# Optimization experiments

Measured on AMD Instinct MI355X. Metric: run time of the kernel, lower is better.

Reference implementation:

```python
import jax, jax.numpy as jnp
import numpy as np

B, T, H, O = 256, 2048, 64, 2


def setup_inputs() -> dict:
    key = jax.random.key(0)
    ks = jax.random.split(key, 14)
    def lin(k, out_f, in_f):
        bound = np.sqrt(6.0 / (in_f + out_f))
        return jax.random.uniform(k, (out_f, in_f), jnp.float32, -bound, bound)
    return {
        "x": jax.random.normal(ks[0], (B, T, 2), jnp.float32),
        "h0": jax.random.normal(ks[1], (1, B, H), jnp.float32),
        "Wa": lin(ks[2], H, H + 1), "ba": jnp.zeros((H,), jnp.float32),
        "Wp1": lin(ks[3], H, H + 1), "bp1": jnp.zeros((H,), jnp.float32),
        "Wp2": lin(ks[4], H, H + 1), "bp2": jnp.zeros((H,), jnp.float32),
        "Wf": lin(ks[5], H, 2 * H), "bf": jnp.zeros((H,), jnp.float32),
        "Wg": lin(ks[6], H, 2 * H), "bg": jnp.zeros((H,), jnp.float32),
        "Wo": lin(ks[7], O, H), "bo": jnp.zeros((O,), jnp.float32),
    }


def reference(x, h0, Wa, ba, Wp1, bp1, Wp2, bp2, Wf, bf, Wg, bg, Wo, bo):
    # x: [B, T, 2] (I/Q), h0: [1, B, H]
    xt = jnp.swapaxes(x, 0, 1)  # [T, B, 2]

    def step(h, x_t):
        i = x_t[:, 0:1]
        q = x_t[:, 1:2]
        amp = jnp.sqrt(i * i + q * q)
        theta = jnp.arctan2(q, i)
        cos_t = jnp.cos(theta)
        sin_t = jnp.sin(theta)
        a = jnp.tanh(jnp.concatenate([h, amp], -1) @ Wa.T + ba)
        p1 = jnp.tanh(jnp.concatenate([h, cos_t], -1) @ Wp1.T + bp1)
        p2 = jnp.tanh(jnp.concatenate([h, sin_t], -1) @ Wp2.T + bp2)
        u = a * p1 * p2 * (1 - a) * (1 - p1) * (1 - p2)
        hu = jnp.concatenate([h, u], -1)
        f = jax.nn.sigmoid(hu @ Wf.T + bf)
        g = jnp.tanh(hu @ Wg.T + bg)
        h_new = f * h + (1 - f) * g
        y = h_new @ Wo.T + bo
        return h_new, y

    _, ys = jax.lax.scan(step, h0[0], xt)  # ys: [T, B, O]
    return jnp.swapaxes(ys, 0, 1)  # [B, T, O]
```

## Files before the change

kernel.cpp:

```cpp
#include <hip/hip_runtime.h>
#include <math.h>

#define BB 256
#define TT 2048
#define HH 64

typedef _Float16 half2v __attribute__((ext_vector_type(2)));
typedef __fp16  fp16v2 __attribute__((ext_vector_type(2)));
union H2I { half2v h; int i; };

#if __has_builtin(__builtin_amdgcn_rcpf)
__device__ __forceinline__ float fast_rcp(float v) { return __builtin_amdgcn_rcpf(v); }
#else
__device__ __forceinline__ float fast_rcp(float v) { return 1.0f / v; }
#endif
#if __has_builtin(__builtin_amdgcn_rsqf)
__device__ __forceinline__ float fast_rsq(float v) { return __builtin_amdgcn_rsqf(v); }
#else
__device__ __forceinline__ float fast_rsq(float v) { return rsqrtf(v); }
#endif

__device__ __forceinline__ float tanh_fast(float v) {
    float e = __expf(2.0f * v);
    return fmaf(-2.0f, fast_rcp(e + 1.0f), 1.0f);
}

__device__ __forceinline__ float sigmoid_fast(float v) {
    return fast_rcp(1.0f + __expf(-v));
}

__device__ __forceinline__ float fdot2(half2v a, half2v b, float c) {
    return __builtin_amdgcn_fdot2(a, b, c, false);
}

__device__ __forceinline__ half2v pack_pair(float a, float b) {
    fp16v2 r = __builtin_amdgcn_cvt_pkrtz(a, b);
    return __builtin_bit_cast(half2v, r);
}

__device__ __forceinline__ void pin_h2(half2v& v) {
    H2I u; u.h = v;
    asm volatile("" : "+v"(u.i));
    v = u.h;
}

__device__ __forceinline__ half2v bcast_pair(half2v v, int lane) {
    H2I u; u.h = v;
    H2I w; w.i = __builtin_amdgcn_readlane(u.i, lane);
    return w.h;
}

__device__ __forceinline__ float dpp_neighbor(float v) {
    return __int_as_float(__builtin_amdgcn_mov_dpp(__float_as_int(v), 0xB1, 0xf, 0xf, true));
}

template <int CTRL>
__device__ __forceinline__ float dpp_add_stage(float v) {
    int t = __builtin_amdgcn_update_dpp(0, __float_as_int(v), CTRL, 0xf, 0xf, true);
    return v + __int_as_float(t);
}

__device__ __forceinline__ float wave_sum_dpp(float v) {
    v = dpp_add_stage<0x111>(v);
    v = dpp_add_stage<0x112>(v);
    v = dpp_add_stage<0x114>(v);
    v = dpp_add_stage<0x118>(v);
    v = dpp_add_stage<0x142>(v);
    v = dpp_add_stage<0x143>(v);
    return v;
}

__global__ __launch_bounds__(256, 1)
void pgjanet_kernel(const float* __restrict__ x,
                    const float* __restrict__ h0,
                    const float* __restrict__ Wa,  const float* __restrict__ ba,
                    const float* __restrict__ Wp1, const float* __restrict__ bp1,
                    const float* __restrict__ Wp2, const float* __restrict__ bp2,
                    const float* __restrict__ Wf,  const float* __restrict__ bf,
                    const float* __restrict__ Wg,  const float* __restrict__ bg,
                    const float* __restrict__ Wo,  const float* __restrict__ bo,
                    float* __restrict__ out)
{
    const int b   = blockIdx.x;
    const int tid = threadIdx.x;
    const int j   = tid & 63;
    const int w   = __builtin_amdgcn_readfirstlane(tid >> 6);

    __shared__ float xs[TT * 2];
    __shared__ float ybuf[TT * 2];
    __shared__ float exch[2][5][HH];

    {
        const float* xp = x + (size_t)b * (TT * 2);
        for (int i = tid; i < TT * 2; i += 256) xs[i] = xp[i];
    }

    const float* gsrc  = (w == 0) ? Wa : (w == 1) ? Wp1 : (w == 2) ? Wp2 : Wf;
    const int    gld   = (w < 3) ? (HH + 1) : (2 * HH);
    const float* g2src = (w == 3) ? Wg : gsrc;
    const int    g2ld  = (w == 3) ? (2 * HH) : gld;

    half2v wgate[32], wgate2[32], wfuv[32], wguv[32];
#pragma unroll
    for (int m = 0; m < 32; ++m) {
        wgate[m]  = pack_pair(gsrc [j * gld  + 2 * m], gsrc [j * gld  + 2 * m + 1]);
        wgate2[m] = pack_pair(g2src[j * g2ld + 2 * m], g2src[j * g2ld + 2 * m + 1]);
        wfuv[m]   = pack_pair(Wf[j * (2 * HH) + HH + 2 * m], Wf[j * (2 * HH) + HH + 2 * m + 1]);
        wguv[m]   = pack_pair(Wg[j * (2 * HH) + HH + 2 * m], Wg[j * (2 * HH) + HH + 2 * m + 1]);
    }
#pragma unroll
    for (int m = 0; m < 32; ++m) {
        pin_h2(wgate[m]); pin_h2(wgate2[m]); pin_h2(wfuv[m]); pin_h2(wguv[m]);
    }

    const float xw   = (w == 0) ? Wa [j * (HH + 1) + HH]
                     : (w == 1) ? Wp1[j * (HH + 1) + HH]
                     : (w == 2) ? Wp2[j * (HH + 1) + HH] : 0.f;
    const float bsel = (w == 0) ? ba[j] : (w == 1) ? bp1[j] : (w == 2) ? bp2[j] : 0.f;
    const float bf_r = bf[j], bg_r = bg[j];
    const float wo0 = Wo[j], wo1 = Wo[HH + j];
    const float bo0 = bo[0], bo1 = bo[1];

    float h = h0[b * HH + j];
    float* yp = out + (size_t)b * (TT * 2);

    __syncthreads();

    float xsel;
    {
        float xi = xs[0], xq = xs[1];
        float r2 = xi * xi + xq * xq;
        float rsq = fast_rsq(r2);
        bool ok = r2 > 0.f;
        float amp = ok ? r2 * rsq : 0.f;
        float ct  = ok ? xi * rsq : 1.f;
        float st  = ok ? xq * rsq : 0.f;
        xsel = (w == 0) ? amp : (w == 1) ? ct : st;
    }

    for (int t = 0; t < TT; ++t) {
        float (*ex)[HH] = exch[t & 1];

        const int tn = (t + 1 < TT) ? (t + 1) : (TT - 1);
        float xi_n = xs[2 * tn], xq_n = xs[2 * tn + 1];
        float xsel_n;
        {
            float r2 = xi_n * xi_n + xq_n * xq_n;
            float rsq = fast_rsq(r2);
            bool ok = r2 > 0.f;
            float amp = ok ? r2 * rsq : 0.f;
            float ct  = ok ? xi_n * rsq : 1.f;
            float st  = ok ? xq_n * rsq : 0.f;
            xsel_n = (w == 0) ? amp : (w == 1) ? ct : st;
        }

        float hnbr = dpp_neighbor(h);
        half2v hp = pack_pair(h, hnbr);
        half2v sh[32];
#pragma unroll
        for (int m = 0; m < 32; ++m) sh[m] = bcast_pair(hp, 2 * m);

        float a0 = 0.f, a1 = 0.f, a2 = 0.f, a3 = 0.f;
#pragma unroll
        for (int m = 0; m < 8; ++m) {
            a0 = fdot2(sh[m],      wgate[m],      a0);
            a1 = fdot2(sh[m + 8],  wgate[m + 8],  a1);
            a2 = fdot2(sh[m + 16], wgate[m + 16], a2);
            a3 = fdot2(sh[m + 24], wgate[m + 24], a3);
        }
        float pre = (a0 + a1) + (a2 + a3);

        if (w == 3) {
            float b0 = 0.f, b1 = 0.f, b2 = 0.f, b3 = 0.f;
#pragma unroll
            for (int m = 0; m < 8; ++m) {
                b0 = fdot2(sh[m],      wgate2[m],      b0);
                b1 = fdot2(sh[m + 8],  wgate2[m + 8],  b1);
                b2 = fdot2(sh[m + 16], wgate2[m + 16], b2);
                b3 = fdot2(sh[m + 24], wgate2[m + 24], b3);
            }
            ex[3][j] = pre + bf_r;
            ex[4][j] = ((b0 + b1) + (b2 + b3)) + bg_r;
        } else {
            ex[w][j] = tanh_fast(pre + fmaf(xsel, xw, bsel));
        }

        __syncthreads();

        float av  = ex[0][j];
        float pv1 = ex[1][j];
        float pv2 = ex[2][j];
        float fh  = ex[3][j];
        float gh  = ex[4][j];
        float u = (av * (1.f - av)) * (pv1 * (1.f - pv1)) * (pv2 * (1.f - pv2));

        float unbr = dpp_neighbor(u);
        half2v upk = pack_pair(u, unbr);
        half2v su[32];
#pragma unroll
        for (int m = 0; m < 32; ++m) su[m] = bcast_pair(upk, 2 * m);

        float f0 = 0.f, f1 = 0.f, f2 = 0.f, f3 = 0.f;
        float g0 = 0.f, g1 = 0.f, g2 = 0.f, g3 = 0.f;
#pragma unroll
        for (int m = 0; m < 8; ++m) {
            f0 = fdot2(su[m],      wfuv[m],      f0);
            f1 = fdot2(su[m + 8],  wfuv[m + 8],  f1);
            f2 = fdot2(su[m + 16], wfuv[m + 16], f2);
            f3 = fdot2(su[m + 24], wfuv[m + 24], f3);
            g0 = fdot2(su[m],      wguv[m],      g0);
            g1 = fdot2(su[m + 8],  wguv[m + 8],  g1);
            g2 = fdot2(su[m + 16], wguv[m + 16], g2);
            g3 = fdot2(su[m + 24], wguv[m + 24], g3);
        }
        float f = sigmoid_fast(fh + (f0 + f1) + (f2 + f3));
        float g = tanh_fast(gh + (g0 + g1) + (g2 + g3));
        h = fmaf(f, h - g, g);

        if (w == (t & 3)) {
            float y0 = wave_sum_dpp(h * wo0);
            float y1 = wave_sum_dpp(h * wo1);
            if (j == 63) {
                ybuf[2 * t]     = y0 + bo0;
                ybuf[2 * t + 1] = y1 + bo1;
            }
        }

        xsel = xsel_n;
    }

    __syncthreads();
    {
        const float4* ys4 = reinterpret_cast<const float4*>(ybuf);
        float4*       yp4 = reinterpret_cast<float4*>(yp);
        for (int i = tid; i < TT * 2 / 4; i += 256) yp4[i] = ys4[i];
    }
}

extern "C" void kernel_launch(void* const* d_in, const int* in_sizes, int n_in,
                              void* d_out, int out_size, void* d_ws, size_t ws_size,
                              hipStream_t stream) {
    const float* x   = (const float*)d_in[0];
    const float* h0  = (const float*)d_in[1];
    const float* Wa  = (const float*)d_in[2];
    const float* ba  = (const float*)d_in[3];
    const float* Wp1 = (const float*)d_in[4];
    const float* bp1 = (const float*)d_in[5];
    const float* Wp2 = (const float*)d_in[6];
    const float* bp2 = (const float*)d_in[7];
    const float* Wf  = (const float*)d_in[8];
    const float* bf  = (const float*)d_in[9];
    const float* Wg  = (const float*)d_in[10];
    const float* bg  = (const float*)d_in[11];
    const float* Wo  = (const float*)d_in[12];
    const float* bo  = (const float*)d_in[13];
    float* out = (float*)d_out;

    pgjanet_kernel<<<dim3(BB), dim3(256), 0, stream>>>(
        x, h0, Wa, ba, Wp1, bp1, Wp2, bp2, Wf, bf, Wg, bg, Wo, bo, out);
}
```

Baseline: 1.511 ms.

## Collapse per-batch work into one wave and remove per-step block barriers

Each batch element now runs in a single 64-thread wave instead of four waves that split the gate matmuls and swapped results through LDS with a __syncthreads every timestep. One wave computes all five h-projections and both u-projections itself, keeping all seven weight matrices in registers. Output projections are deferred: h is buffered in LDS and every 64 steps each lane computes one timestep's outputs, writing them straight to global memory. This removes the per-step barrier and LDS exchange, but puts more serial dot-product work on each wave, with higher register pressure and less parallelism per CU.

```diff
diff --git a/kernel.cpp b/kernel.cpp
--- a/kernel.cpp
+++ b/kernel.cpp
@@ -54,23 +54,7 @@
     return __int_as_float(__builtin_amdgcn_mov_dpp(__float_as_int(v), 0xB1, 0xf, 0xf, true));
 }
 
-template <int CTRL>
-__device__ __forceinline__ float dpp_add_stage(float v) {
-    int t = __builtin_amdgcn_update_dpp(0, __float_as_int(v), CTRL, 0xf, 0xf, true);
-    return v + __int_as_float(t);
-}
-
-__device__ __forceinline__ float wave_sum_dpp(float v) {
-    v = dpp_add_stage<0x111>(v);
-    v = dpp_add_stage<0x112>(v);
-    v = dpp_add_stage<0x114>(v);
-    v = dpp_add_stage<0x118>(v);
-    v = dpp_add_stage<0x142>(v);
-    v = dpp_add_stage<0x143>(v);
-    return v;
-}
-
-__global__ __launch_bounds__(256, 1)
+__global__ __launch_bounds__(64, 1)
 void pgjanet_kernel(const float* __restrict__ x,
                     const float* __restrict__ h0,
                     const float* __restrict__ Wa,  const float* __restrict__ ba,
@@ -81,159 +65,137 @@
                     const float* __restrict__ Wo,  const float* __restrict__ bo,
                     float* __restrict__ out)
 {
-    const int b   = blockIdx.x;
-    const int tid = threadIdx.x;
-    const int j   = tid & 63;
-    const int w   = __builtin_amdgcn_readfirstlane(tid >> 6);
+    const int b = blockIdx.x;
+    const int j = threadIdx.x;
 
     __shared__ float xs[TT * 2];
-    __shared__ float ybuf[TT * 2];
-    __shared__ float exch[2][5][HH];
+    __shared__ float hbuf[64][HH + 1];
+    __shared__ float woLDS[2 * HH];
 
     {
-        const float* xp = x + (size_t)b * (TT * 2);
-        for (int i = tid; i < TT * 2; i += 256) xs[i] = xp[i];
-    }
-
-    const float* gsrc  = (w == 0) ? Wa : (w == 1) ? Wp1 : (w == 2) ? Wp2 : Wf;
-    const int    gld   = (w < 3) ? (HH + 1) : (2 * HH);
-    const float* g2src = (w == 3) ? Wg : gsrc;
-    const int    g2ld  = (w == 3) ? (2 * HH) : gld;
-
-    half2v wgate[32], wgate2[32], wfuv[32], wguv[32];
-#pragma unroll
-    for (int m = 0; m < 32; ++m) {
-        wgate[m]  = pack_pair(gsrc [j * gld  + 2 * m], gsrc [j * gld  + 2 * m + 1]);
-        wgate2[m] = pack_pair(g2src[j * g2ld + 2 * m], g2src[j * g2ld + 2 * m + 1]);
-        wfuv[m]   = pack_pair(Wf[j * (2 * HH) + HH + 2 * m], Wf[j * (2 * HH) + HH + 2 * m + 1]);
-        wguv[m]   = pack_pair(Wg[j * (2 * HH) + HH + 2 * m], Wg[j * (2 * HH) + HH + 2 * m + 1]);
-    }
-#pragma unroll
-    for (int m = 0; m < 32; ++m) {
-        pin_h2(wgate[m]); pin_h2(wgate2[m]); pin_h2(wfuv[m]); pin_h2(wguv[m]);
-    }
-
-    const float xw   = (w == 0) ? Wa [j * (HH + 1) + HH]
-                     : (w == 1) ? Wp1[j * (HH + 1) + HH]
-                     : (w == 2) ? Wp2[j * (HH + 1) + HH] : 0.f;
-    const float bsel = (w == 0) ? ba[j] : (w == 1) ? bp1[j] : (w == 2) ? bp2[j] : 0.f;
+        const float4* xp4 = reinterpret_cast<const float4*>(x + (size_t)b * (TT * 2));
+        float4*       xs4 = reinterpret_cast<float4*>(xs);
+#pragma unroll
+        for (int i = 0; i < (TT * 2 / 4) / 64; ++i) xs4[j + 64 * i] = xp4[j + 64 * i];
+    }
+    for (int i = j; i < 2 * HH; i += 64) woLDS[i] = Wo[i];
+
+    half2v w5[5][32], wfu[32], wgu[32];
+    {
+        const float* Wsrc[5] = {Wa, Wp1, Wp2, Wf, Wg};
+        const int    ldv[5]  = {HH + 1, HH + 1, HH + 1, 2 * HH, 2 * HH};
+#pragma unroll
+        for (int g = 0; g < 5; ++g) {
+            const float* r = Wsrc[g] + (size_t)j * ldv[g];
+#pragma unroll
+            for (int m = 0; m < 32; ++m) w5[g][m] = pack_pair(r[2 * m], r[2 * m + 1]);
+        }
+        const float* rf = Wf + (size_t)j * (2 * HH) + HH;
+        const float* rg = Wg + (size_t)j * (2 * HH) + HH;
+#pragma unroll
+        for (int m = 0; m < 32; ++m) {
+            wfu[m] = pack_pair(rf[2 * m], rf[2 * m + 1]);
+            wgu[m] = pack_pair(rg[2 * m], rg[2 * m + 1]);
+        }
+#pragma unroll
+        for (int g = 0; g < 5; ++g)
+#pragma unroll
+            for (int m = 0; m < 32; ++m) pin_h2(w5[g][m]);
+#pragma unroll
+        for (int m = 0; m < 32; ++m) { pin_h2(wfu[m]); pin_h2(wgu[m]); }
+    }
+
+    const float waX  = Wa [j * (HH + 1) + HH];
+    const float wp1X = Wp1[j * (HH + 1) + HH];
+    const float wp2X = Wp2[j * (HH + 1) + HH];
+    const float ba_r = ba[j], bp1_r = bp1[j], bp2_r = bp2[j];
     const float bf_r = bf[j], bg_r = bg[j];
-    const float wo0 = Wo[j], wo1 = Wo[HH + j];
-    const float bo0 = bo[0], bo1 = bo[1];
-
-    float h = h0[b * HH + j];
+    const float bo0  = bo[0], bo1 = bo[1];
+
+    float  h  = h0[b * HH + j];
     float* yp = out + (size_t)b * (TT * 2);
 
     __syncthreads();
 
-    float xsel;
+    float amp, ct, st;
     {
         float xi = xs[0], xq = xs[1];
         float r2 = xi * xi + xq * xq;
-        float rsq = fast_rsq(r2);
+        float rq = fast_rsq(r2);
         bool ok = r2 > 0.f;
-        float amp = ok ? r2 * rsq : 0.f;
-        float ct  = ok ? xi * rsq : 1.f;
-        float st  = ok ? xq * rsq : 0.f;
-        xsel = (w == 0) ? amp : (w == 1) ? ct : st;
+        amp = ok ? r2 * rq : 0.f;
+        ct  = ok ? xi * rq : 1.f;
+        st  = ok ? xq * rq : 0.f;
     }
 
     for (int t = 0; t < TT; ++t) {
-        float (*ex)[HH] = exch[t & 1];
-
-        const int tn = (t + 1 < TT) ? (t + 1) : (TT - 1);
+        const int tn = (t + 1 < TT) ? (t + 1) : t;
         float xi_n = xs[2 * tn], xq_n = xs[2 * tn + 1];
-        float xsel_n;
+        float amp_n, ct_n, st_n;
         {
             float r2 = xi_n * xi_n + xq_n * xq_n;
-            float rsq = fast_rsq(r2);
+            float rq = fast_rsq(r2);
             bool ok = r2 > 0.f;
-            float amp = ok ? r2 * rsq : 0.f;
-            float ct  = ok ? xi_n * rsq : 1.f;
-            float st  = ok ? xq_n * rsq : 0.f;
-            xsel_n = (w == 0) ? amp : (w == 1) ? ct : st;
-        }
-
-        float hnbr = dpp_neighbor(h);
-        half2v hp = pack_pair(h, hnbr);
+            amp_n = ok ? r2 * rq : 0.f;
+            ct_n  = ok ? xi_n * rq : 1.f;
+            st_n  = ok ? xq_n * rq : 0.f;
+        }
+
+        float  hnbr = dpp_neighbor(h);
+        half2v hp   = pack_pair(h, hnbr);
         half2v sh[32];
 #pragma unroll
         for (int m = 0; m < 32; ++m) sh[m] = bcast_pair(hp, 2 * m);
 
-        float a0 = 0.f, a1 = 0.f, a2 = 0.f, a3 = 0.f;
-#pragma unroll
-        for (int m = 0; m < 8; ++m) {
-            a0 = fdot2(sh[m],      wgate[m],      a0);
-            a1 = fdot2(sh[m + 8],  wgate[m + 8],  a1);
-            a2 = fdot2(sh[m + 16], wgate[m + 16], a2);
-            a3 = fdot2(sh[m + 24], wgate[m + 24], a3);
-        }
-        float pre = (a0 + a1) + (a2 + a3);
-
-        if (w == 3) {
-            float b0 = 0.f, b1 = 0.f, b2 = 0.f, b3 = 0.f;
-#pragma unroll
-            for (int m = 0; m < 8; ++m) {
-                b0 = fdot2(sh[m],      wgate2[m],      b0);
-                b1 = fdot2(sh[m + 8],  wgate2[m + 8],  b1);
-                b2 = fdot2(sh[m + 16], wgate2[m + 16], b2);
-                b3 = fdot2(sh[m + 24], wgate2[m + 24], b3);
+        float acc[5];
+        acc[0] = fmaf(amp, waX,  ba_r);
+        acc[1] = fmaf(ct,  wp1X, bp1_r);
+        acc[2] = fmaf(st,  wp2X, bp2_r);
+        acc[3] = bf_r;
+        acc[4] = bg_r;
+#pragma unroll
+        for (int m = 0; m < 32; ++m)
+#pragma unroll
+            for (int g = 0; g < 5; ++g)
+                acc[g] = fdot2(sh[m], w5[g][m], acc[g]);
+
+        float av = tanh_fast(acc[0]);
+        float p1 = tanh_fast(acc[1]);
+        float p2 = tanh_fast(acc[2]);
+        float u = fmaf(-av, av, av) * fmaf(-p1, p1, p1) * fmaf(-p2, p2, p2);
+
+        float  unbr = dpp_neighbor(u);
+        half2v up   = pack_pair(u, unbr);
+        half2v su[32];
+#pragma unroll
+        for (int m = 0; m < 32; ++m) su[m] = bcast_pair(up, 2 * m);
+
+        float f0 = acc[3], f1 = 0.f, g0 = acc[4], g1 = 0.f;
+#pragma unroll
+        for (int m = 0; m < 16; ++m) {
+            f0 = fdot2(su[m],      wfu[m],      f0);
+            f1 = fdot2(su[m + 16], wfu[m + 16], f1);
+            g0 = fdot2(su[m],      wgu[m],      g0);
+            g1 = fdot2(su[m + 16], wgu[m + 16], g1);
+        }
+        float f = sigmoid_fast(f0 + f1);
+        float g = tanh_fast(g0 + g1);
+        h = fmaf(f, h - g, g);
+
+        hbuf[t & 63][j] = h;
+
+        if ((t & 63) == 63) {
+            float y0 = bo0, y1 = bo1;
+#pragma unroll 4
+            for (int k = 0; k < HH; ++k) {
+                float hv = hbuf[j][k];
+                y0 = fmaf(hv, woLDS[k],      y0);
+                y1 = fmaf(hv, woLDS[HH + k], y1);
             }
-            ex[3][j] = pre + bf_r;
-            ex[4][j] = ((b0 + b1) + (b2 + b3)) + bg_r;
-        } else {
-            ex[w][j] = tanh_fast(pre + fmaf(xsel, xw, bsel));
-        }
-
-        __syncthreads();
-
-        float av  = ex[0][j];
-        float pv1 = ex[1][j];
-        float pv2 = ex[2][j];
-        float fh  = ex[3][j];
-        float gh  = ex[4][j];
-        float u = (av * (1.f - av)) * (pv1 * (1.f - pv1)) * (pv2 * (1.f - pv2));
-
-        float unbr = dpp_neighbor(u);
-        half2v upk = pack_pair(u, unbr);
-        half2v su[32];
-#pragma unroll
-        for (int m = 0; m < 32; ++m) su[m] = bcast_pair(upk, 2 * m);
-
-        float f0 = 0.f, f1 = 0.f, f2 = 0.f, f3 = 0.f;
-        float g0 = 0.f, g1 = 0.f, g2 = 0.f, g3 = 0.f;
-#pragma unroll
-        for (int m = 0; m < 8; ++m) {
-            f0 = fdot2(su[m],      wfuv[m],      f0);
-            f1 = fdot2(su[m + 8],  wfuv[m + 8],  f1);
-            f2 = fdot2(su[m + 16], wfuv[m + 16], f2);
-            f3 = fdot2(su[m + 24], wfuv[m + 24], f3);
-            g0 = fdot2(su[m],      wguv[m],      g0);
-            g1 = fdot2(su[m + 8],  wguv[m + 8],  g1);
-            g2 = fdot2(su[m + 16], wguv[m + 16], g2);
-            g3 = fdot2(su[m + 24], wguv[m + 24], g3);
-        }
-        float f = sigmoid_fast(fh + (f0 + f1) + (f2 + f3));
-        float g = tanh_fast(gh + (g0 + g1) + (g2 + g3));
-        h = fmaf(f, h - g, g);
-
-        if (w == (t & 3)) {
-            float y0 = wave_sum_dpp(h * wo0);
-            float y1 = wave_sum_dpp(h * wo1);
-            if (j == 63) {
-                ybuf[2 * t]     = y0 + bo0;
-                ybuf[2 * t + 1] = y1 + bo1;
-            }
-        }
-
-        xsel = xsel_n;
-    }
-
-    __syncthreads();
-    {
-        const float4* ys4 = reinterpret_cast<const float4*>(ybuf);
-        float4*       yp4 = reinterpret_cast<float4*>(yp);
-        for (int i = tid; i < TT * 2 / 4; i += 256) yp4[i] = ys4[i];
+            reinterpret_cast<float2*>(yp)[(t - 63) + j] = make_float2(y0, y1);
+        }
+
+        amp = amp_n; ct = ct_n; st = st_n;
     }
 }
 
@@ -256,6 +218,6 @@
     const float* bo  = (const float*)d_in[13];
     float* out = (float*)d_out;
 
-    pgjanet_kernel<<<dim3(BB), dim3(256), 0, stream>>>(
+    pgjanet_kernel<<<dim3(BB), dim3(64), 0, stream>>>(
         x, h0, Wa, ba, Wp1, bp1, Wp2, bp2, Wf, bf, Wg, bg, Wo, bo, out);
 }
```

New measurement: 1.478 ms. -2.1%, faster.
